# Kernel optimization log

Measured on AMD Instinct MI355X. Metric: run time of the kernel, lower is better.

The kernel has to match this reference:

```python
import jax, jax.numpy as jnp
import numpy as np

V = 128          # vocab_size
S = 32           # sentence_size
E = 16           # embedding_size
M = 128          # memory_size
L = 128          # linear_output_size
B = 16
N = 127


def _position_encoding(sentence_size, embedding_size):
    enc = np.ones((embedding_size, sentence_size), dtype=np.float32)
    ls = sentence_size + 1
    le = embedding_size + 1
    for i in range(1, le):
        for j in range(1, ls):
            enc[i - 1, j - 1] = (i - (le - 1) / 2) * (j - (ls - 1) / 2)
    enc = 1 + 4 * enc / embedding_size / sentence_size
    return enc.T  # [S, E]


def setup_inputs() -> dict:
    key = jax.random.key(0)
    ks = jax.random.split(key, 12)
    node_fts = jax.random.randint(ks[0], (B, N, S), 0, V).astype(jnp.float32)
    edge_fts = jax.random.randint(ks[1], (B, N, N, S), 0, V).astype(jnp.float32)
    graph_fts = jax.random.randint(ks[2], (B, S), 0, V).astype(jnp.float32)
    adj_mat = jax.random.randint(ks[3], (B, N, N), 0, 2).astype(jnp.float32)
    hidden = jnp.zeros((B, N, E), jnp.float32)
    sc = 0.02
    query_biases = sc * jax.random.normal(ks[4], (V - 1, E), jnp.float32)
    stories_biases = sc * jax.random.normal(ks[5], (V - 1, E), jnp.float32)
    output_biases = sc * jax.random.normal(ks[6], (V - 1, E), jnp.float32)
    memory_contents = sc * jax.random.normal(ks[7], (M, E), jnp.float32)
    W_int = sc * jax.random.normal(ks[8], (E, E), jnp.float32)   # intermediate_linear (unused, num_hops=1)
    W_out = sc * jax.random.normal(ks[9], (E, L), jnp.float32)   # output_linear
    W_fin = sc * jax.random.normal(ks[10], (L, V), jnp.float32)  # final_linear
    enc = jnp.asarray(_position_encoding(S, E))
    return dict(node_fts=node_fts, edge_fts=edge_fts, graph_fts=graph_fts,
                adj_mat=adj_mat, hidden=hidden, enc=enc,
                query_biases=query_biases, stories_biases=stories_biases,
                output_biases=output_biases, memory_contents=memory_contents,
                W_int=W_int, W_out=W_out, W_fin=W_fin)


def reference(node_fts, edge_fts, graph_fts, adj_mat, hidden, enc,
              query_biases, stories_biases, output_biases, memory_contents,
              W_int, W_out, W_fin):
    del hidden
    b, n, s = node_fts.shape
    # [B, N+1, S]: nodes plus graph feature row
    naf = jnp.concatenate([node_fts, graph_fts[:, None, :]], axis=1)
    # mask edges then pad to [B, N+1, N+1, S]
    ef = edge_fts * adj_mat[..., None]
    ef = jnp.pad(ef, ((0, 0), (0, 1), (0, 1), (0, 0)))
    bt = b * (n + 1)
    queries = naf.reshape(bt, s)                 # [BT, S]
    stories = ef.reshape(bt, n + 1, s)           # [BT, M0, S], M0 = N+1

    nil = jnp.zeros((1, enc.shape[1]), queries.dtype)
    sb = jnp.concatenate([stories_biases, nil], axis=0)   # [V, E]
    qb = jnp.concatenate([query_biases, nil], axis=0)
    ob = jnp.concatenate([output_biases, nil], axis=0)

    sidx = jnp.maximum(stories.astype(jnp.int32), 0)       # clamp_min(0)
    qidx = jnp.maximum(queries.astype(jnp.int32), 0)

    # position-encoded weighted sums over the sentence axis
    mem = jnp.einsum('bmse,se->bme', sb[sidx], enc)        # [BT, M0, E]
    Cj = jnp.einsum('bmse,se->bme', ob[sidx], enc)         # [BT, M0, E]
    pad_m = memory_contents.shape[0] - (n + 1)
    mem = jnp.pad(mem, ((0, 0), (0, pad_m), (0, 0))) + memory_contents
    Cj = jnp.pad(Cj, ((0, 0), (0, pad_m), (0, 0)))
    u = jnp.einsum('bse,se->be', qb[qidx], enc)            # [BT, E]

    # num_hops = 1
    x = u
    probs = jax.nn.softmax(jnp.einsum('bme,be->bm', mem, x), axis=-1)
    o = jnp.einsum('bme,bm->be', Cj, probs)
    x = jax.nn.relu((x + o) @ W_out)                       # last hop -> output_linear + relu
    ret = x @ W_fin                                        # [BT, V]

    nxt = ret.reshape(b, n + 1, -1)
    return nxt[:, :-1, :] + nxt[:, -1:, :]                 # [B, N, V]
```

## Files before the change

kernel.cpp:

```cpp
#include <hip/hip_runtime.h>

#define Vn 128
#define Sn 32
#define En 16
#define M0 128
#define Ln 128
#define Bn 16
#define Nn 127
#define BTn 2048
#define RS 20

__global__ __launch_bounds__(256, 4) void memnet_main(
    const float* __restrict__ node_fts, const float* __restrict__ edge_fts,
    const float* __restrict__ graph_fts, const float* __restrict__ adjm,
    const float* __restrict__ enc, const float* __restrict__ qb,
    const float* __restrict__ sb, const float* __restrict__ ob,
    const float* __restrict__ mc, const float* __restrict__ wout,
    const float* __restrict__ wfin, float* __restrict__ ret)
{
    __shared__ __align__(16) float sbL[M0 * RS];
    __shared__ __align__(16) float obL[M0 * RS];
    __shared__ __align__(16) float encL[Sn * En];
    __shared__ unsigned int idxw[M0 * 8];
    __shared__ float cjT[En * 129];
    __shared__ float scoresL[M0];
    __shared__ float probsL[M0];
    __shared__ float opart[128];
    __shared__ float uL[En];
    __shared__ float uoL[En];
    __shared__ float xL[Ln];
    __shared__ float red[8];

    const int t = threadIdx.x;
    const int bt = blockIdx.x;
    const int b = bt >> 7;
    const int i = bt & 127;

    for (int c = t; c < 512; c += 256) {
        int r = c >> 2, q = c & 3;
        float4 v = make_float4(0.f, 0.f, 0.f, 0.f);
        float4 w = make_float4(0.f, 0.f, 0.f, 0.f);
        if (r < 127) {
            v = *(const float4*)&sb[r * 16 + q * 4];
            w = *(const float4*)&ob[r * 16 + q * 4];
        }
        *(float4*)&sbL[r * RS + q * 4] = v;
        *(float4*)&obL[r * RS + q * 4] = w;
    }
    if (t < 128) {
        *(float4*)&encL[t * 4] = *(const float4*)&enc[t * 4];
    }
    for (int c = t; c < 1024; c += 256) {
        int m = c >> 3, q = c & 7;
        unsigned int packed = 0u;
        if (i < 127 && m < 127) {
            float a = adjm[(b * 127 + i) * 127 + m];
            if (a != 0.f) {
                const float4 v = *(const float4*)&edge_fts[(size_t)(((b * 127 + i) * 127 + m)) * 32 + q * 4];
                packed = (unsigned)(int)v.x | ((unsigned)(int)v.y << 8)
                       | ((unsigned)(int)v.z << 16) | ((unsigned)(int)v.w << 24);
            }
        }
        idxw[m * 8 + q] = packed;
    }
    if (t < 16) {
        float ue = 0.f;
        for (int s = 0; s < 32; s++) {
            float qv = (i < 127) ? node_fts[(b * 127 + i) * 32 + s] : graph_fts[b * 32 + s];
            int qi = (int)qv;
            if (qi < 0) qi = 0;
            float w = (qi < 127) ? qb[qi * 16 + t] : 0.f;
            ue = fmaf(w, enc[s * 16 + t], ue);
        }
        uL[t] = ue;
    }
    __syncthreads();

    const int eg4 = (t & 3) * 4;
    const int md = t >> 2;
    const int m0 = md;
    const int m1 = md + 64;

    float4 aM0 = make_float4(0.f, 0.f, 0.f, 0.f);
    float4 aM1 = make_float4(0.f, 0.f, 0.f, 0.f);
    float4 aC0 = make_float4(0.f, 0.f, 0.f, 0.f);
    float4 aC1 = make_float4(0.f, 0.f, 0.f, 0.f);

    for (int sq = 0; sq < 8; sq++) {
        unsigned w0 = idxw[m0 * 8 + sq];
        unsigned w1 = idxw[m1 * 8 + sq];
#pragma unroll
        for (int j = 0; j < 4; j++) {
            int s = sq * 4 + j;
            int i0 = (w0 >> (8 * j)) & 0xFF;
            int i1 = (w1 >> (8 * j)) & 0xFF;
            float4 eb = *(const float4*)&encL[s * 16 + eg4];
            float4 a0 = *(const float4*)&sbL[i0 * RS + eg4];
            float4 c0 = *(const float4*)&obL[i0 * RS + eg4];
            float4 a1 = *(const float4*)&sbL[i1 * RS + eg4];
            float4 c1 = *(const float4*)&obL[i1 * RS + eg4];
            aM0.x = fmaf(a0.x, eb.x, aM0.x); aM0.y = fmaf(a0.y, eb.y, aM0.y);
            aM0.z = fmaf(a0.z, eb.z, aM0.z); aM0.w = fmaf(a0.w, eb.w, aM0.w);
            aC0.x = fmaf(c0.x, eb.x, aC0.x); aC0.y = fmaf(c0.y, eb.y, aC0.y);
            aC0.z = fmaf(c0.z, eb.z, aC0.z); aC0.w = fmaf(c0.w, eb.w, aC0.w);
            aM1.x = fmaf(a1.x, eb.x, aM1.x); aM1.y = fmaf(a1.y, eb.y, aM1.y);
            aM1.z = fmaf(a1.z, eb.z, aM1.z); aM1.w = fmaf(a1.w, eb.w, aM1.w);
            aC1.x = fmaf(c1.x, eb.x, aC1.x); aC1.y = fmaf(c1.y, eb.y, aC1.y);
            aC1.z = fmaf(c1.z, eb.z, aC1.z); aC1.w = fmaf(c1.w, eb.w, aC1.w);
        }
    }

    {
        float4 u4 = *(const float4*)&uL[eg4];
        float4 mc0 = *(const float4*)&mc[m0 * 16 + eg4];
        float4 mc1 = *(const float4*)&mc[m1 * 16 + eg4];
        float p0 = (aM0.x + mc0.x) * u4.x + (aM0.y + mc0.y) * u4.y
                 + (aM0.z + mc0.z) * u4.z + (aM0.w + mc0.w) * u4.w;
        float p1 = (aM1.x + mc1.x) * u4.x + (aM1.y + mc1.y) * u4.y
                 + (aM1.z + mc1.z) * u4.z + (aM1.w + mc1.w) * u4.w;
        p0 += __shfl_xor(p0, 1); p0 += __shfl_xor(p0, 2);
        p1 += __shfl_xor(p1, 1); p1 += __shfl_xor(p1, 2);
        if ((t & 3) == 0) { scoresL[m0] = p0; scoresL[m1] = p1; }
        cjT[(eg4 + 0) * 129 + m0] = aC0.x; cjT[(eg4 + 1) * 129 + m0] = aC0.y;
        cjT[(eg4 + 2) * 129 + m0] = aC0.z; cjT[(eg4 + 3) * 129 + m0] = aC0.w;
        cjT[(eg4 + 0) * 129 + m1] = aC1.x; cjT[(eg4 + 1) * 129 + m1] = aC1.y;
        cjT[(eg4 + 2) * 129 + m1] = aC1.z; cjT[(eg4 + 3) * 129 + m1] = aC1.w;
    }
    __syncthreads();

    {
        float v = (t < 128) ? scoresL[t] : -1e30f;
#pragma unroll
        for (int off = 32; off > 0; off >>= 1) v = fmaxf(v, __shfl_xor(v, off));
        if ((t & 63) == 0) red[t >> 6] = v;
        __syncthreads();
        float mx = fmaxf(fmaxf(red[0], red[1]), fmaxf(red[2], red[3]));
        float ex = (t < 128) ? __expf(scoresL[t] - mx) : 0.f;
        float sv = ex;
#pragma unroll
        for (int off = 32; off > 0; off >>= 1) sv += __shfl_xor(sv, off);
        __syncthreads();
        if ((t & 63) == 0) red[t >> 6] = sv;
        __syncthreads();
        float sum = red[0] + red[1] + red[2] + red[3];
        if (t < 128) probsL[t] = ex / sum;
    }
    __syncthreads();

    if (t < 128) {
        int e = t & 15, ch = t >> 4;
        float acc = 0.f;
#pragma unroll
        for (int k = 0; k < 16; k++) {
            int m = ch * 16 + k;
            acc = fmaf(probsL[m], cjT[e * 129 + m], acc);
        }
        opart[t] = acc;
    }
    __syncthreads();
    if (t < 16) {
        float o = 0.f;
#pragma unroll
        for (int ch = 0; ch < 8; ch++) o += opart[ch * 16 + t];
        uoL[t] = uL[t] + o;
    }
    __syncthreads();

    if (t < 128) {
        float acc = 0.f;
#pragma unroll
        for (int e = 0; e < 16; e++) acc = fmaf(uoL[e], wout[e * 128 + t], acc);
        xL[t] = fmaxf(acc, 0.f);
    }
    __syncthreads();
    if (t < 128) {
        float acc = 0.f;
        for (int l = 0; l < 128; l++) acc = fmaf(xL[l], wfin[l * 128 + t], acc);
        ret[bt * 128 + t] = acc;
    }
}

__global__ void memnet_out(const float* __restrict__ ret, float* __restrict__ out)
{
    int idx = blockIdx.x * 256 + threadIdx.x;
    if (idx >= Bn * Nn * Vn) return;
    int v = idx & 127;
    int r = idx >> 7;
    int b = r / 127;
    int i = r - b * 127;
    out[idx] = ret[(b * 128 + i) * 128 + v] + ret[(b * 128 + 127) * 128 + v];
}

extern "C" void kernel_launch(void* const* d_in, const int* in_sizes, int n_in,
                              void* d_out, int out_size, void* d_ws, size_t ws_size,
                              hipStream_t stream)
{
    const float* node  = (const float*)d_in[0];
    const float* edge  = (const float*)d_in[1];
    const float* graph = (const float*)d_in[2];
    const float* adjm  = (const float*)d_in[3];
    const float* enc   = (const float*)d_in[5];
    const float* qb    = (const float*)d_in[6];
    const float* sb    = (const float*)d_in[7];
    const float* ob    = (const float*)d_in[8];
    const float* mc    = (const float*)d_in[9];
    const float* wout  = (const float*)d_in[11];
    const float* wfin  = (const float*)d_in[12];

    float* ws = (float*)d_ws;

    memnet_main<<<BTn, 256, 0, stream>>>(node, edge, graph, adjm, enc, qb,
                                         sb, ob, mc, wout, wfin, ws);
    const int total = Bn * Nn * Vn;
    memnet_out<<<(total + 255) / 256, 256, 0, stream>>>(ws, (float*)d_out);
}
```

Before: 132.4 us.

## Compact active adjacency slots and compute masked memory rows analytically

Uses a ballot over the adjacency row to build a compact list of active memory slots. Edge features are loaded and the position-encoded gather is computed only for those slots. Masked slots (all indices zero) get a closed-form score and output contribution from a precomputed constant. The final linear layer is also split across all 256 threads with a shared-memory reduction. This roughly halves the gather and compute work, at the cost of extra syncs and index bookkeeping.

```diff
diff --git a/kernel.cpp b/kernel.cpp
--- a/kernel.cpp
+++ b/kernel.cpp
@@ -1,10 +1,6 @@
 #include <hip/hip_runtime.h>
 
 #define Vn 128
-#define Sn 32
-#define En 16
-#define M0 128
-#define Ln 128
 #define Bn 16
 #define Nn 127
 #define BTn 2048
@@ -18,18 +14,23 @@
     const float* __restrict__ mc, const float* __restrict__ wout,
     const float* __restrict__ wfin, float* __restrict__ ret)
 {
-    __shared__ __align__(16) float sbL[M0 * RS];
-    __shared__ __align__(16) float obL[M0 * RS];
-    __shared__ __align__(16) float encL[Sn * En];
-    __shared__ unsigned int idxw[M0 * 8];
-    __shared__ float cjT[En * 129];
-    __shared__ float scoresL[M0];
-    __shared__ float probsL[M0];
+    __shared__ __align__(16) float sbL[128 * RS];
+    __shared__ __align__(16) float obL[128 * RS];
+    __shared__ __align__(16) float encL[32 * 16];
+    __shared__ __align__(16) unsigned idxc[128 * 8];
+    __shared__ float cjT[16 * 129];
+    __shared__ float scoresL[128];
+    __shared__ float probsL[128];
+    __shared__ float probC[128];
     __shared__ float opart[128];
-    __shared__ float uL[En];
-    __shared__ float uoL[En];
-    __shared__ float xL[Ln];
-    __shared__ float red[8];
+    __shared__ float xL[128];
+    __shared__ int actmL[128];
+    __shared__ unsigned char actF[128];
+    __shared__ __align__(16) float uL[16];
+    __shared__ float uoL[16], cCL[16];
+    __shared__ float red[4];
+    __shared__ unsigned long long wmaskL[4];
+    __shared__ float k0L;
 
     const int t = threadIdx.x;
     const int bt = blockIdx.x;
@@ -47,84 +48,86 @@
         *(float4*)&sbL[r * RS + q * 4] = v;
         *(float4*)&obL[r * RS + q * 4] = w;
     }
-    if (t < 128) {
-        *(float4*)&encL[t * 4] = *(const float4*)&enc[t * 4];
-    }
-    for (int c = t; c < 1024; c += 256) {
-        int m = c >> 3, q = c & 7;
-        unsigned int packed = 0u;
-        if (i < 127 && m < 127) {
-            float a = adjm[(b * 127 + i) * 127 + m];
-            if (a != 0.f) {
-                const float4 v = *(const float4*)&edge_fts[(size_t)(((b * 127 + i) * 127 + m)) * 32 + q * 4];
-                packed = (unsigned)(int)v.x | ((unsigned)(int)v.y << 8)
-                       | ((unsigned)(int)v.z << 16) | ((unsigned)(int)v.w << 24);
-            }
-        }
-        idxw[m * 8 + q] = packed;
+    if (t < 128) *(float4*)&encL[t * 4] = *(const float4*)&enc[t * 4];
+    bool act = false;
+    if (t < 127 && i < 127) act = (adjm[(b * 127 + i) * 127 + t] != 0.f);
+    unsigned long long bal = __ballot(act);
+    if ((t & 63) == 0) wmaskL[t >> 6] = bal;
+    if (t < 128) actF[t] = act ? 1 : 0;
+    __syncthreads();
+
+    const int nact = (int)(__popcll(wmaskL[0]) + __popcll(wmaskL[1]));
+    if (act) {
+        int wid = t >> 6;
+        int base = (wid == 1) ? (int)__popcll(wmaskL[0]) : 0;
+        int pos = base + (int)__popcll(wmaskL[wid] & ((1ull << (t & 63)) - 1ull));
+        actmL[pos] = t;
     }
     if (t < 16) {
+        float es = 0.f;
+#pragma unroll
+        for (int s = 0; s < 32; s++) es += encL[s * 16 + t];
         float ue = 0.f;
         for (int s = 0; s < 32; s++) {
             float qv = (i < 127) ? node_fts[(b * 127 + i) * 32 + s] : graph_fts[b * 32 + s];
-            int qi = (int)qv;
-            if (qi < 0) qi = 0;
+            int qi = (int)qv; if (qi < 0) qi = 0;
             float w = (qi < 127) ? qb[qi * 16 + t] : 0.f;
-            ue = fmaf(w, enc[s * 16 + t], ue);
+            ue = fmaf(w, encL[s * 16 + t], ue);
         }
         uL[t] = ue;
+        cCL[t] = obL[t] * es;
+        float kv = sbL[t] * es * ue;
+        kv += __shfl_xor(kv, 1); kv += __shfl_xor(kv, 2);
+        kv += __shfl_xor(kv, 4); kv += __shfl_xor(kv, 8);
+        if (t == 0) k0L = kv;
+    }
+    __syncthreads();
+
+    const int n8 = nact * 8;
+    for (int c = t; c < n8; c += 256) {
+        int m = actmL[c >> 3], q = c & 7;
+        const float4 v = *(const float4*)&edge_fts[(((size_t)(b * 127 + i)) * 127 + m) * 32 + q * 4];
+        idxc[c] = (unsigned)(int)v.x | ((unsigned)(int)v.y << 8)
+                | ((unsigned)(int)v.z << 16) | ((unsigned)(int)v.w << 24);
+    }
+    if (t < 128) {
+        float mdot = 0.f;
+#pragma unroll
+        for (int e = 0; e < 16; e++) mdot = fmaf(mc[t * 16 + e], uL[e], mdot);
+        scoresL[t] = mdot + (actF[t] ? 0.f : k0L);
     }
     __syncthreads();
 
     const int eg4 = (t & 3) * 4;
     const int md = t >> 2;
-    const int m0 = md;
-    const int m1 = md + 64;
-
-    float4 aM0 = make_float4(0.f, 0.f, 0.f, 0.f);
-    float4 aM1 = make_float4(0.f, 0.f, 0.f, 0.f);
-    float4 aC0 = make_float4(0.f, 0.f, 0.f, 0.f);
-    float4 aC1 = make_float4(0.f, 0.f, 0.f, 0.f);
-
-    for (int sq = 0; sq < 8; sq++) {
-        unsigned w0 = idxw[m0 * 8 + sq];
-        unsigned w1 = idxw[m1 * 8 + sq];
-#pragma unroll
-        for (int j = 0; j < 4; j++) {
-            int s = sq * 4 + j;
-            int i0 = (w0 >> (8 * j)) & 0xFF;
-            int i1 = (w1 >> (8 * j)) & 0xFF;
-            float4 eb = *(const float4*)&encL[s * 16 + eg4];
-            float4 a0 = *(const float4*)&sbL[i0 * RS + eg4];
-            float4 c0 = *(const float4*)&obL[i0 * RS + eg4];
-            float4 a1 = *(const float4*)&sbL[i1 * RS + eg4];
-            float4 c1 = *(const float4*)&obL[i1 * RS + eg4];
-            aM0.x = fmaf(a0.x, eb.x, aM0.x); aM0.y = fmaf(a0.y, eb.y, aM0.y);
-            aM0.z = fmaf(a0.z, eb.z, aM0.z); aM0.w = fmaf(a0.w, eb.w, aM0.w);
-            aC0.x = fmaf(c0.x, eb.x, aC0.x); aC0.y = fmaf(c0.y, eb.y, aC0.y);
-            aC0.z = fmaf(c0.z, eb.z, aC0.z); aC0.w = fmaf(c0.w, eb.w, aC0.w);
-            aM1.x = fmaf(a1.x, eb.x, aM1.x); aM1.y = fmaf(a1.y, eb.y, aM1.y);
-            aM1.z = fmaf(a1.z, eb.z, aM1.z); aM1.w = fmaf(a1.w, eb.w, aM1.w);
-            aC1.x = fmaf(c1.x, eb.x, aC1.x); aC1.y = fmaf(c1.y, eb.y, aC1.y);
-            aC1.z = fmaf(c1.z, eb.z, aC1.z); aC1.w = fmaf(c1.w, eb.w, aC1.w);
-        }
-    }
-
-    {
-        float4 u4 = *(const float4*)&uL[eg4];
-        float4 mc0 = *(const float4*)&mc[m0 * 16 + eg4];
-        float4 mc1 = *(const float4*)&mc[m1 * 16 + eg4];
-        float p0 = (aM0.x + mc0.x) * u4.x + (aM0.y + mc0.y) * u4.y
-                 + (aM0.z + mc0.z) * u4.z + (aM0.w + mc0.w) * u4.w;
-        float p1 = (aM1.x + mc1.x) * u4.x + (aM1.y + mc1.y) * u4.y
-                 + (aM1.z + mc1.z) * u4.z + (aM1.w + mc1.w) * u4.w;
-        p0 += __shfl_xor(p0, 1); p0 += __shfl_xor(p0, 2);
-        p1 += __shfl_xor(p1, 1); p1 += __shfl_xor(p1, 2);
-        if ((t & 3) == 0) { scoresL[m0] = p0; scoresL[m1] = p1; }
-        cjT[(eg4 + 0) * 129 + m0] = aC0.x; cjT[(eg4 + 1) * 129 + m0] = aC0.y;
-        cjT[(eg4 + 2) * 129 + m0] = aC0.z; cjT[(eg4 + 3) * 129 + m0] = aC0.w;
-        cjT[(eg4 + 0) * 129 + m1] = aC1.x; cjT[(eg4 + 1) * 129 + m1] = aC1.y;
-        cjT[(eg4 + 2) * 129 + m1] = aC1.z; cjT[(eg4 + 3) * 129 + m1] = aC1.w;
+    const float4 u4 = *(const float4*)&uL[eg4];
+    for (int kk = md; kk < nact; kk += 64) {
+        int m = actmL[kk];
+        float4 aM = make_float4(0.f, 0.f, 0.f, 0.f);
+        float4 aC = make_float4(0.f, 0.f, 0.f, 0.f);
+#pragma unroll
+        for (int sq = 0; sq < 8; sq++) {
+            unsigned w = idxc[kk * 8 + sq];
+#pragma unroll
+            for (int j = 0; j < 4; j++) {
+                int s = sq * 4 + j;
+                int ix = (int)((w >> (8 * j)) & 0xFF);
+                float4 eb = *(const float4*)&encL[s * 16 + eg4];
+                float4 a  = *(const float4*)&sbL[ix * RS + eg4];
+                float4 cc = *(const float4*)&obL[ix * RS + eg4];
+                aM.x = fmaf(a.x, eb.x, aM.x); aM.y = fmaf(a.y, eb.y, aM.y);
+                aM.z = fmaf(a.z, eb.z, aM.z); aM.w = fmaf(a.w, eb.w, aM.w);
+                aC.x = fmaf(cc.x, eb.x, aC.x); aC.y = fmaf(cc.y, eb.y, aC.y);
+                aC.z = fmaf(cc.z, eb.z, aC.z); aC.w = fmaf(cc.w, eb.w, aC.w);
+            }
+        }
+        float p = aM.x * u4.x + aM.y * u4.y + aM.z * u4.z + aM.w * u4.w;
+        p += __shfl_xor(p, 1); p += __shfl_xor(p, 2);
+        if ((t & 3) == 0) scoresL[m] += p;
+        cjT[(eg4 + 0) * 129 + kk] = aC.x;
+        cjT[(eg4 + 1) * 129 + kk] = aC.y;
+        cjT[(eg4 + 2) * 129 + kk] = aC.z;
+        cjT[(eg4 + 3) * 129 + kk] = aC.w;
     }
     __syncthreads();
 
@@ -147,14 +150,23 @@
     }
     __syncthreads();
 
+    {
+        float pa = 0.f;
+        if (t < 128) {
+            pa = (t < nact) ? probsL[actmL[t]] : 0.f;
+            probC[t] = pa;
+        }
+        float sv = pa;
+#pragma unroll
+        for (int off = 32; off > 0; off >>= 1) sv += __shfl_xor(sv, off);
+        if ((t & 63) == 0) red[t >> 6] = sv;
+    }
+    __syncthreads();
+
     if (t < 128) {
         int e = t & 15, ch = t >> 4;
         float acc = 0.f;
-#pragma unroll
-        for (int k = 0; k < 16; k++) {
-            int m = ch * 16 + k;
-            acc = fmaf(probsL[m], cjT[e * 129 + m], acc);
-        }
+        for (int k = ch; k < nact; k += 8) acc += probC[k] * cjT[e * 129 + k];
         opart[t] = acc;
     }
     __syncthreads();
@@ -162,7 +174,8 @@
         float o = 0.f;
 #pragma unroll
         for (int ch = 0; ch < 8; ch++) o += opart[ch * 16 + t];
-        uoL[t] = uL[t] + o;
+        float sumAct = red[0] + red[1] + red[2] + red[3];
+        uoL[t] = uL[t] + o + cCL[t] * (1.f - sumAct);
     }
     __syncthreads();
 
@@ -173,11 +186,20 @@
         xL[t] = fmaxf(acc, 0.f);
     }
     __syncthreads();
-    if (t < 128) {
+
+    float* part = sbL;
+    {
+        int v = t & 127, h = t >> 7;
         float acc = 0.f;
-        for (int l = 0; l < 128; l++) acc = fmaf(xL[l], wfin[l * 128 + t], acc);
-        ret[bt * 128 + t] = acc;
-    }
+#pragma unroll
+        for (int l0 = 0; l0 < 64; l0++) {
+            int l = h * 64 + l0;
+            acc = fmaf(xL[l], wfin[l * 128 + v], acc);
+        }
+        part[t] = acc;
+    }
+    __syncthreads();
+    if (t < 128) ret[bt * 128 + t] = part[t] + part[t + 128];
 }
 
 __global__ void memnet_out(const float* __restrict__ ret, float* __restrict__ out)
```

New measurement: 269.6 us. +103.7%, slower.
